# Kernel optimization log

Hardware: AMD Instinct MI355X
Metric: run time of the kernel (lower is better)

Reference implementation:

```python
import jax, jax.numpy as jnp
import numpy as np

DN = ('NCHW', 'OIHW', 'NCHW')


def conv2d(x, w, b, pad=1):
    y = jax.lax.conv_general_dilated(x, w, window_strides=(1, 1),
                                     padding=[(pad, pad), (pad, pad)],
                                     dimension_numbers=DN)
    return y + b[None, :, None, None]


def deform_conv2d(x, offset, w, b):
    """Deformable conv v1 (torchvision layout): offset [B, 2*K*K, H, W],
    channel 2k = dy_k, 2k+1 = dx_k, kernel points row-major."""
    B, C, H, W = x.shape
    K = 3
    off = offset.reshape(B, K * K, 2, H, W)
    dy, dx = off[:, :, 0], off[:, :, 1]            # [B,9,H,W]
    ky = jnp.repeat(jnp.arange(K) - 1, K).astype(x.dtype)   # row-major kernel grid
    kx = jnp.tile(jnp.arange(K) - 1, K).astype(x.dtype)
    hh = jnp.arange(H, dtype=x.dtype)
    ww = jnp.arange(W, dtype=x.dtype)
    py = hh[None, None, :, None] + ky[None, :, None, None] + dy  # [B,9,H,W]
    px = ww[None, None, None, :] + kx[None, :, None, None] + dx

    y0 = jnp.floor(py)
    x0 = jnp.floor(px)
    ly, lx = py - y0, px - x0
    y0i, x0i = y0.astype(jnp.int32), x0.astype(jnp.int32)

    def gather(yi, xi):
        valid = ((yi >= 0) & (yi < H) & (xi >= 0) & (xi < W))
        yc = jnp.clip(yi, 0, H - 1)
        xc = jnp.clip(xi, 0, W - 1)
        # per-batch fancy gather: [C,H,W] indexed by [9,H,W] -> [C,9,H,W]
        g = jax.vmap(lambda xb, yy, xx: xb[:, yy, xx])(x, yc, xc)  # [B,C,9,H,W]
        return g * valid[:, None].astype(x.dtype)

    w00 = ((1 - ly) * (1 - lx))[:, None]
    w01 = ((1 - ly) * lx)[:, None]
    w10 = (ly * (1 - lx))[:, None]
    w11 = (ly * lx)[:, None]
    val = (gather(y0i, x0i) * w00 + gather(y0i, x0i + 1) * w01 +
           gather(y0i + 1, x0i) * w10 + gather(y0i + 1, x0i + 1) * w11)  # [B,C,9,H,W]

    wk = w.reshape(w.shape[0], C * K * K)                 # [Cout, C*9]
    out = jnp.einsum('bkhw,ok->bohw', val.reshape(B, C * K * K, H, W), wk)
    return out + b[None, :, None, None]


def setup_inputs() -> dict:
    key = jax.random.key(0)
    k1, k2, k3, k4 = jax.random.split(key, 4)
    B, Cin, Cout, H, W = 8, 128, 256, 64, 64
    fan = 1.0 / np.sqrt(Cin * 9)
    return {
        'x': jax.random.normal(k1, (B, Cin, H, W), jnp.float32),
        'w_off': jax.random.normal(k2, (18, Cin, 3, 3), jnp.float32) * 0.01,
        'b_off': jnp.zeros((18,), jnp.float32),
        'w_def': jax.random.normal(k3, (Cout, Cin, 3, 3), jnp.float32) * fan,
        'b_def': jax.random.normal(k4, (Cout,), jnp.float32) * 0.01,
    }


def reference(x, w_off, b_off, w_def, b_def):
    offset = conv2d(x, w_off, b_off, pad=1)
    y = deform_conv2d(x, offset, w_def, b_def)
    return jax.nn.relu(y)
```

## Files before the change

kernel.cpp:

```cpp
#include <hip/hip_runtime.h>
#include <hip/hip_bf16.h>

#define HH 64
#define WW 64
#define CIN 128
#define COUT 256
#define KK 1152
#define PW 66
#define XTIMG (PW*PW*CIN)

typedef short bf16x8 __attribute__((ext_vector_type(8)));
typedef float f32x4  __attribute__((ext_vector_type(4)));

__device__ inline short f2bf(float f) {
    union { float f; unsigned u; } v; v.f = f;
    unsigned r = v.u + 0x7FFFu + ((v.u >> 16) & 1u);
    return (short)(r >> 16);
}
__device__ inline float lo16(unsigned u) {
    union { unsigned u; float f; } v; v.u = u << 16; return v.f;
}
__device__ inline float hi16(unsigned u) {
    union { unsigned u; float f; } v; v.u = u & 0xffff0000u; return v.f;
}
__device__ inline unsigned pk2(float lo, float hi) {
    union { __hip_bfloat162 h; unsigned u; } c;
    c.h = __float22bfloat162_rn(make_float2(lo, hi));
    return c.u;
}

__global__ __launch_bounds__(256) void prep(const float* __restrict__ x,
                                            const float* __restrict__ wd,
                                            const float* __restrict__ wo,
                                            ushort* __restrict__ xt,
                                            short* __restrict__ wf,
                                            short* __restrict__ wfo) {
    int bi = blockIdx.x, t = threadIdx.x;
    if (bi < 528) {
        int b = bi & 7, hp = bi >> 3;
        ushort* row = xt + ((size_t)b * PW + hp) * PW * CIN;
        if (hp == 0 || hp == 65) {
            uint4 z = {0, 0, 0, 0};
            for (int f = t; f < 1056; f += 256) ((uint4*)row)[f] = z;
            return;
        }
        int h = hp - 1;
        int w = t & 63, c0 = (t >> 6) * 32;
        const float* xs = x + (((size_t)b * CIN + c0) << 12) + (h << 6) + w;
        float v[32];
#pragma unroll
        for (int i = 0; i < 32; i++) v[i] = xs[(size_t)i << 12];
        unsigned dw[16];
#pragma unroll
        for (int i = 0; i < 16; i++) dw[i] = pk2(v[2 * i], v[2 * i + 1]);
        ushort* dst = row + ((w + 1) * 128 + c0);
#pragma unroll
        for (int i = 0; i < 4; i++) *(uint4*)(dst + i * 8) = *(uint4*)&dw[i * 4];
        if (t < 32) {
            uint4 z = {0, 0, 0, 0};
            int px = (t >> 4) * 65;
            *(uint4*)(row + px * 128 + (t & 15) * 8) = z;
        }
        return;
    }
    int flat = (bi - 528) * 256 + t;
    int m = flat / 2304;
    int r = flat - m * 2304;
    int ks = r >> 6, l = r & 63;
    bf16x8 v8;
    if (m < 16) {
        int co = m * 16 + (l & 15);
#pragma unroll
        for (int j = 0; j < 8; j++) {
            int ckp = ks * 32 + ((l >> 4) << 3) + j;
            int c = ckp & 127, k = ckp >> 7;
            v8[j] = f2bf(wd[(size_t)co * KK + c * 9 + k]);
        }
        *(bf16x8*)(wf + ((size_t)(m * 36 + ks) * 64 + l) * 8) = v8;
    } else {
        int mm = m - 16;
        int co = mm * 16 + (l & 15);
#pragma unroll
        for (int j = 0; j < 8; j++) {
            int ckp = ks * 32 + ((l >> 4) << 3) + j;
            int c = ckp & 127, k = ckp >> 7;
            v8[j] = (co < 18) ? f2bf(wo[(size_t)co * KK + c * 9 + k]) : (short)0;
        }
        *(bf16x8*)(wfo + ((size_t)(mm * 36 + ks) * 64 + l) * 8) = v8;
    }
}

__global__ __launch_bounds__(512, 4) void fused_deform(const ushort* __restrict__ xt,
                                                       const short* __restrict__ wf,
                                                       const short* __restrict__ wfo,
                                                       const float* __restrict__ bo,
                                                       const float* __restrict__ bias,
                                                       float* __restrict__ out) {
    __shared__ short   s_val[2][64][128];
    __shared__ float4  s_w[9][64];
    __shared__ ushort2 s_o[9][64];
    __shared__ float   s_off[18][64];

    int t = threadIdx.x, bi = blockIdx.x;
    int b = bi & 7, h = bi >> 3;
    const ushort* xb = xt + (size_t)b * XTIMG;
    int wv = t >> 6, l = t & 63, lane16 = l & 15, quad = l >> 4;

    {
        int mt = wv >> 2, nt = wv & 3;
        int pix0 = nt * 16 + lane16;
        f32x4 aoff = {0.f, 0.f, 0.f, 0.f};
        const short* A = wfo + (size_t)mt * 36 * 512 + l * 8;
#pragma unroll
        for (int k = 0; k < 9; k++) {
            const ushort* bbase = xb + ((size_t)(h + k / 3) * PW + pix0 + k % 3) * CIN + quad * 8;
#pragma unroll
            for (int ksp = 0; ksp < 4; ksp++) {
                bf16x8 bfr = *(const bf16x8*)(bbase + ksp * 32);
                bf16x8 afr = *(const bf16x8*)(A + (k * 4 + ksp) * 512);
                aoff = __builtin_amdgcn_mfma_f32_16x16x32_bf16(afr, bfr, aoff, 0, 0, 0);
            }
        }
#pragma unroll
        for (int r = 0; r < 4; r++) {
            int co = mt * 16 + quad * 4 + r;
            if (co < 18) s_off[co][pix0] = aoff[r] + bo[co];
        }
    }
    __syncthreads();

    for (int jj = t; jj < 576; jj += 512) {
        int k = jj >> 6, pixj = jj & 63;
        float dy = s_off[2 * k][pixj];
        float dx = s_off[2 * k + 1][pixj];
        float py = (float)(h + k / 3 - 1) + dy;
        float px = (float)(pixj + k % 3 - 1) + dx;
        float y0f = floorf(py), x0f = floorf(px);
        float ly = py - y0f, lx = px - x0f;
        int y0 = (int)y0f, x0 = (int)x0f;
        float a0, a1;
        if (x0 >= 0 && x0 <= 62)      { a0 = 1.f - lx; a1 = lx; }
        else if (x0 == -1)            { a0 = lx;       a1 = 0.f; }
        else if (x0 == 63)            { a0 = 0.f;      a1 = 1.f - lx; }
        else                          { a0 = 0.f;      a1 = 0.f; }
        int xb0 = min(max(x0, 0), 62);
        bool vy0 = (y0 >= 0) && (y0 < HH);
        bool vy1 = (y0 >= -1) && (y0 < HH - 1);
        int y0c = min(max(y0, 0), HH - 1);
        int y1c = min(max(y0 + 1, 0), HH - 1);
        float wy0 = (1.f - ly) * (vy0 ? 1.f : 0.f);
        float wy1 = ly * (vy1 ? 1.f : 0.f);
        s_o[k][pixj] = make_ushort2((ushort)((y0c + 1) * PW + xb0 + 1),
                                    (ushort)((y1c + 1) * PW + xb0 + 1));
        s_w[k][pixj] = make_float4(wy0 * a0, wy0 * a1, wy1 * a0, wy1 * a1);
    }

    int p = t >> 3, j = t & 7, c0 = j * 16;
    int g0 = ((2 * j) ^ (p & 15)) * 8, g1 = ((2 * j + 1) ^ (p & 15)) * 8;
    bf16x8 rv[8];
    auto gload = [&](int k) {
        ushort2 o = s_o[k][p];
        const ushort* p0 = xb + (size_t)o.x * CIN + c0;
        const ushort* p1 = xb + (size_t)o.y * CIN + c0;
        rv[0] = *(const bf16x8*)(p0);       rv[1] = *(const bf16x8*)(p0 + 8);
        rv[2] = *(const bf16x8*)(p0 + 128); rv[3] = *(const bf16x8*)(p0 + 136);
        rv[4] = *(const bf16x8*)(p1);       rv[5] = *(const bf16x8*)(p1 + 8);
        rv[6] = *(const bf16x8*)(p1 + 128); rv[7] = *(const bf16x8*)(p1 + 136);
    };
    auto gstore = [&](int k, int buf) {
        float4 w4 = s_w[k][p];
        unsigned oa[4], ob[4];
        const unsigned* u0 = (const unsigned*)&rv[0];
        const unsigned* u2 = (const unsigned*)&rv[2];
        const unsigned* u4 = (const unsigned*)&rv[4];
        const unsigned* u6 = (const unsigned*)&rv[6];
        const unsigned* u1 = (const unsigned*)&rv[1];
        const unsigned* u3 = (const unsigned*)&rv[3];
        const unsigned* u5 = (const unsigned*)&rv[5];
        const unsigned* u7 = (const unsigned*)&rv[7];
#pragma unroll
        for (int d = 0; d < 4; d++) {
            float vl = w4.x * lo16(u0[d]) + w4.y * lo16(u2[d]) + w4.z * lo16(u4[d]) + w4.w * lo16(u6[d]);
            float vh = w4.x * hi16(u0[d]) + w4.y * hi16(u2[d]) + w4.z * hi16(u4[d]) + w4.w * hi16(u6[d]);
            oa[d] = pk2(vl, vh);
            float wl = w4.x * lo16(u1[d]) + w4.y * lo16(u3[d]) + w4.z * lo16(u5[d]) + w4.w * lo16(u7[d]);
            float wh = w4.x * hi16(u1[d]) + w4.y * hi16(u3[d]) + w4.z * hi16(u5[d]) + w4.w * hi16(u7[d]);
            ob[d] = pk2(wl, wh);
        }
        *(bf16x8*)&s_val[buf][p][g0] = *(bf16x8*)oa;
        *(bf16x8*)&s_val[buf][p][g1] = *(bf16x8*)ob;
    };

    f32x4 z = {0.f, 0.f, 0.f, 0.f};
    f32x4 acc[2][4];
#pragma unroll
    for (int i = 0; i < 2; i++)
#pragma unroll
        for (int jj2 = 0; jj2 < 4; jj2++) acc[i][jj2] = z;
    const short* Aw = wf + (size_t)l * 8 + (size_t)(wv * 2) * 36 * 512;

    __syncthreads();
    gload(0); gstore(0, 0);
    __syncthreads();

    for (int k = 0; k < 9; k++) {
        if (k < 8) gload(k + 1);
#pragma unroll
        for (int ksp = 0; ksp < 4; ksp++) {
            int ks = k * 4 + ksp;
            int gsw = ((ksp * 4 + quad) ^ lane16) * 8;
            bf16x8 b0 = *(const bf16x8*)&s_val[k & 1][lane16     ][gsw];
            bf16x8 b1 = *(const bf16x8*)&s_val[k & 1][16 + lane16][gsw];
            bf16x8 b2 = *(const bf16x8*)&s_val[k & 1][32 + lane16][gsw];
            bf16x8 b3 = *(const bf16x8*)&s_val[k & 1][48 + lane16][gsw];
            bf16x8 a0 = *(const bf16x8*)(Aw + (size_t)(0 * 36 + ks) * 512);
            bf16x8 a1 = *(const bf16x8*)(Aw + (size_t)(1 * 36 + ks) * 512);
            acc[0][0] = __builtin_amdgcn_mfma_f32_16x16x32_bf16(a0, b0, acc[0][0], 0, 0, 0);
            acc[0][1] = __builtin_amdgcn_mfma_f32_16x16x32_bf16(a0, b1, acc[0][1], 0, 0, 0);
            acc[0][2] = __builtin_amdgcn_mfma_f32_16x16x32_bf16(a0, b2, acc[0][2], 0, 0, 0);
            acc[0][3] = __builtin_amdgcn_mfma_f32_16x16x32_bf16(a0, b3, acc[0][3], 0, 0, 0);
            acc[1][0] = __builtin_amdgcn_mfma_f32_16x16x32_bf16(a1, b0, acc[1][0], 0, 0, 0);
            acc[1][1] = __builtin_amdgcn_mfma_f32_16x16x32_bf16(a1, b1, acc[1][1], 0, 0, 0);
            acc[1][2] = __builtin_amdgcn_mfma_f32_16x16x32_bf16(a1, b2, acc[1][2], 0, 0, 0);
            acc[1][3] = __builtin_amdgcn_mfma_f32_16x16x32_bf16(a1, b3, acc[1][3], 0, 0, 0);
        }
        if (k < 8) gstore(k + 1, (k + 1) & 1);
        __syncthreads();
    }

#pragma unroll
    for (int mt2 = 0; mt2 < 2; mt2++) {
        int co = (wv * 2 + mt2) * 16 + quad * 4;
#pragma unroll
        for (int nt = 0; nt < 4; nt++) {
            int colx = nt * 16 + lane16;
#pragma unroll
            for (int rr = 0; rr < 4; rr++) {
                float v = acc[mt2][nt][rr] + bias[co + rr];
                out[(((size_t)b * COUT + co + rr) << 12) + (h << 6) + colx] = fmaxf(v, 0.f);
            }
        }
    }
}

extern "C" void kernel_launch(void* const* d_in, const int* in_sizes, int n_in,
                              void* d_out, int out_size, void* d_ws, size_t ws_size,
                              hipStream_t stream) {
    const float* x     = (const float*)d_in[0];
    const float* w_off = (const float*)d_in[1];
    const float* b_off = (const float*)d_in[2];
    const float* w_def = (const float*)d_in[3];
    const float* b_def = (const float*)d_in[4];
    float* out = (float*)d_out;

    short*  wf  = (short*)d_ws;
    short*  wfo = wf + (size_t)16 * 36 * 512;
    ushort* xt  = (ushort*)(wfo + (size_t)2 * 36 * 512);

    prep<<<690, 256, 0, stream>>>(x, w_def, w_off, xt, wf, wfo);
    fused_deform<<<512, 512, 0, stream>>>(xt, wf, wfo, b_off, b_def, out);
}
```

Before: 135.0 us.

## Process two kernel taps per pipeline stage to halve block barriers

Restructures the gather/MFMA pipeline so each stage gathers and interpolates two kernel taps into a 64x256 shared tile, then runs eight K-slices per stage. This cuts the number of __syncthreads from nine to five and gives each load batch a longer compute window to hide latency behind. Shared memory is now one manually carved buffer, with s_off aliased onto the value buffer, and grows to about 77 KB. The extra shared memory and the 16-register gather buffer may reduce blocks per CU. Per-thread channel assignment also changes to strided 8-element chunks.

```diff
diff --git a/kernel.cpp b/kernel.cpp
--- a/kernel.cpp
+++ b/kernel.cpp
@@ -96,10 +96,11 @@
                                                        const float* __restrict__ bo,
                                                        const float* __restrict__ bias,
                                                        float* __restrict__ out) {
-    __shared__ short   s_val[2][64][128];
-    __shared__ float4  s_w[9][64];
-    __shared__ ushort2 s_o[9][64];
-    __shared__ float   s_off[18][64];
+    __shared__ __align__(16) char smem[77056];
+    short*   s_val = (short*)smem;
+    float*   s_off = (float*)smem;
+    float4*  s_w   = (float4*)(smem + 65536);
+    ushort2* s_o   = (ushort2*)(smem + 65536 + 9216);
 
     int t = threadIdx.x, bi = blockIdx.x;
     int b = bi & 7, h = bi >> 3;
@@ -124,15 +125,15 @@
 #pragma unroll
         for (int r = 0; r < 4; r++) {
             int co = mt * 16 + quad * 4 + r;
-            if (co < 18) s_off[co][pix0] = aoff[r] + bo[co];
+            if (co < 18) s_off[co * 64 + pix0] = aoff[r] + bo[co];
         }
     }
     __syncthreads();
 
     for (int jj = t; jj < 576; jj += 512) {
         int k = jj >> 6, pixj = jj & 63;
-        float dy = s_off[2 * k][pixj];
-        float dx = s_off[2 * k + 1][pixj];
+        float dy = s_off[(2 * k) * 64 + pixj];
+        float dx = s_off[(2 * k + 1) * 64 + pixj];
         float py = (float)(h + k / 3 - 1) + dy;
         float px = (float)(pixj + k % 3 - 1) + dx;
         float y0f = floorf(py), x0f = floorf(px);
@@ -150,45 +151,46 @@
         int y1c = min(max(y0 + 1, 0), HH - 1);
         float wy0 = (1.f - ly) * (vy0 ? 1.f : 0.f);
         float wy1 = ly * (vy1 ? 1.f : 0.f);
-        s_o[k][pixj] = make_ushort2((ushort)((y0c + 1) * PW + xb0 + 1),
-                                    (ushort)((y1c + 1) * PW + xb0 + 1));
-        s_w[k][pixj] = make_float4(wy0 * a0, wy0 * a1, wy1 * a0, wy1 * a1);
-    }
-
-    int p = t >> 3, j = t & 7, c0 = j * 16;
-    int g0 = ((2 * j) ^ (p & 15)) * 8, g1 = ((2 * j + 1) ^ (p & 15)) * 8;
-    bf16x8 rv[8];
-    auto gload = [&](int k) {
-        ushort2 o = s_o[k][p];
-        const ushort* p0 = xb + (size_t)o.x * CIN + c0;
-        const ushort* p1 = xb + (size_t)o.y * CIN + c0;
-        rv[0] = *(const bf16x8*)(p0);       rv[1] = *(const bf16x8*)(p0 + 8);
-        rv[2] = *(const bf16x8*)(p0 + 128); rv[3] = *(const bf16x8*)(p0 + 136);
-        rv[4] = *(const bf16x8*)(p1);       rv[5] = *(const bf16x8*)(p1 + 8);
-        rv[6] = *(const bf16x8*)(p1 + 128); rv[7] = *(const bf16x8*)(p1 + 136);
+        s_o[k * 64 + pixj] = make_ushort2((ushort)((y0c + 1) * PW + xb0 + 1),
+                                          (ushort)((y1c + 1) * PW + xb0 + 1));
+        s_w[k * 64 + pixj] = make_float4(wy0 * a0, wy0 * a1, wy1 * a0, wy1 * a1);
+    }
+
+    int p = t >> 3, j = t & 7, pm = p & 15, jj8 = j * 8;
+    bf16x8 rv[16];
+
+    auto gld = [&](int k, bf16x8* r) {
+        ushort2 o = s_o[k * 64 + p];
+        const ushort* q0 = xb + (size_t)o.x * CIN + jj8;
+        const ushort* q1 = xb + (size_t)o.y * CIN + jj8;
+        r[0] = *(const bf16x8*)(q0);       r[1] = *(const bf16x8*)(q0 + 64);
+        r[2] = *(const bf16x8*)(q0 + 128); r[3] = *(const bf16x8*)(q0 + 192);
+        r[4] = *(const bf16x8*)(q1);       r[5] = *(const bf16x8*)(q1 + 64);
+        r[6] = *(const bf16x8*)(q1 + 128); r[7] = *(const bf16x8*)(q1 + 192);
     };
-    auto gstore = [&](int k, int buf) {
-        float4 w4 = s_w[k][p];
+    auto gst = [&](int k, int buf, bf16x8* r) {
+        float4 w4 = s_w[k * 64 + p];
         unsigned oa[4], ob[4];
-        const unsigned* u0 = (const unsigned*)&rv[0];
-        const unsigned* u2 = (const unsigned*)&rv[2];
-        const unsigned* u4 = (const unsigned*)&rv[4];
-        const unsigned* u6 = (const unsigned*)&rv[6];
-        const unsigned* u1 = (const unsigned*)&rv[1];
-        const unsigned* u3 = (const unsigned*)&rv[3];
-        const unsigned* u5 = (const unsigned*)&rv[5];
-        const unsigned* u7 = (const unsigned*)&rv[7];
+        const unsigned* cA0 = (const unsigned*)&r[0];
+        const unsigned* cA1 = (const unsigned*)&r[2];
+        const unsigned* cA2 = (const unsigned*)&r[4];
+        const unsigned* cA3 = (const unsigned*)&r[6];
+        const unsigned* cB0 = (const unsigned*)&r[1];
+        const unsigned* cB1 = (const unsigned*)&r[3];
+        const unsigned* cB2 = (const unsigned*)&r[5];
+        const unsigned* cB3 = (const unsigned*)&r[7];
 #pragma unroll
         for (int d = 0; d < 4; d++) {
-            float vl = w4.x * lo16(u0[d]) + w4.y * lo16(u2[d]) + w4.z * lo16(u4[d]) + w4.w * lo16(u6[d]);
-            float vh = w4.x * hi16(u0[d]) + w4.y * hi16(u2[d]) + w4.z * hi16(u4[d]) + w4.w * hi16(u6[d]);
+            float vl = w4.x * lo16(cA0[d]) + w4.y * lo16(cA1[d]) + w4.z * lo16(cA2[d]) + w4.w * lo16(cA3[d]);
+            float vh = w4.x * hi16(cA0[d]) + w4.y * hi16(cA1[d]) + w4.z * hi16(cA2[d]) + w4.w * hi16(cA3[d]);
             oa[d] = pk2(vl, vh);
-            float wl = w4.x * lo16(u1[d]) + w4.y * lo16(u3[d]) + w4.z * lo16(u5[d]) + w4.w * lo16(u7[d]);
-            float wh = w4.x * hi16(u1[d]) + w4.y * hi16(u3[d]) + w4.z * hi16(u5[d]) + w4.w * hi16(u7[d]);
-            ob[d] = pk2(wl, wh);
-        }
-        *(bf16x8*)&s_val[buf][p][g0] = *(bf16x8*)oa;
-        *(bf16x8*)&s_val[buf][p][g1] = *(bf16x8*)ob;
+            float ul = w4.x * lo16(cB0[d]) + w4.y * lo16(cB1[d]) + w4.z * lo16(cB2[d]) + w4.w * lo16(cB3[d]);
+            float uh = w4.x * hi16(cB0[d]) + w4.y * hi16(cB1[d]) + w4.z * hi16(cB2[d]) + w4.w * hi16(cB3[d]);
+            ob[d] = pk2(ul, uh);
+        }
+        short* base = s_val + buf * 16384 + p * 256 + (k & 1) * 128;
+        *(bf16x8*)(base + ((j    ) ^ pm) * 8) = *(bf16x8*)oa;
+        *(bf16x8*)(base + ((j + 8) ^ pm) * 8) = *(bf16x8*)ob;
     };
 
     f32x4 z = {0.f, 0.f, 0.f, 0.f};
@@ -196,23 +198,29 @@
 #pragma unroll
     for (int i = 0; i < 2; i++)
 #pragma unroll
-        for (int jj2 = 0; jj2 < 4; jj2++) acc[i][jj2] = z;
+        for (int q2 = 0; q2 < 4; q2++) acc[i][q2] = z;
     const short* Aw = wf + (size_t)l * 8 + (size_t)(wv * 2) * 36 * 512;
 
     __syncthreads();
-    gload(0); gstore(0, 0);
+    gld(0, rv); gld(1, rv + 8);
+    gst(0, 0, rv); gst(1, 0, rv + 8);
     __syncthreads();
 
-    for (int k = 0; k < 9; k++) {
-        if (k < 8) gload(k + 1);
-#pragma unroll
-        for (int ksp = 0; ksp < 4; ksp++) {
-            int ks = k * 4 + ksp;
-            int gsw = ((ksp * 4 + quad) ^ lane16) * 8;
-            bf16x8 b0 = *(const bf16x8*)&s_val[k & 1][lane16     ][gsw];
-            bf16x8 b1 = *(const bf16x8*)&s_val[k & 1][16 + lane16][gsw];
-            bf16x8 b2 = *(const bf16x8*)&s_val[k & 1][32 + lane16][gsw];
-            bf16x8 b3 = *(const bf16x8*)&s_val[k & 1][48 + lane16][gsw];
+#pragma unroll 1
+    for (int s = 0; s < 5; s++) {
+        int kn = 2 * s + 2;
+        if (kn <= 8) gld(kn, rv);
+        if (kn + 1 <= 8) gld(kn + 1, rv + 8);
+        const short* sv = s_val + (s & 1) * 16384;
+        int nk = (s == 4) ? 4 : 8;
+#pragma unroll 4
+        for (int ksp = 0; ksp < nk; ksp++) {
+            int ks = s * 8 + ksp;
+            int colg = (((ksp & 3) * 4 + quad) ^ lane16) * 8 + (ksp >> 2) * 128;
+            bf16x8 b0 = *(const bf16x8*)(sv + (lane16     ) * 256 + colg);
+            bf16x8 b1 = *(const bf16x8*)(sv + (lane16 + 16) * 256 + colg);
+            bf16x8 b2 = *(const bf16x8*)(sv + (lane16 + 32) * 256 + colg);
+            bf16x8 b3 = *(const bf16x8*)(sv + (lane16 + 48) * 256 + colg);
             bf16x8 a0 = *(const bf16x8*)(Aw + (size_t)(0 * 36 + ks) * 512);
             bf16x8 a1 = *(const bf16x8*)(Aw + (size_t)(1 * 36 + ks) * 512);
             acc[0][0] = __builtin_amdgcn_mfma_f32_16x16x32_bf16(a0, b0, acc[0][0], 0, 0, 0);
@@ -224,8 +232,9 @@
             acc[1][2] = __builtin_amdgcn_mfma_f32_16x16x32_bf16(a1, b2, acc[1][2], 0, 0, 0);
             acc[1][3] = __builtin_amdgcn_mfma_f32_16x16x32_bf16(a1, b3, acc[1][3], 0, 0, 0);
         }
-        if (k < 8) gstore(k + 1, (k + 1) & 1);
-        __syncthreads();
+        if (kn <= 8) gst(kn, (s + 1) & 1, rv);
+        if (kn + 1 <= 8) gst(kn + 1, (s + 1) & 1, rv + 8);
+        if (s < 4) __syncthreads();
     }
 
 #pragma unroll
```

After: 163.8 us. 1.21x slower.
